# Kernel optimization log

Hardware: AMD Instinct MI355X
Metric: run time of the kernel (lower is better)

## Reference

```python
import jax, jax.numpy as jnp
import numpy as np

B, P, N = 512, 30, 60
S, NV = 14, 5
HID, DE, DO, NT = 64, 5, 6, 2


def _lin(key, out_d, in_d):
    k1, k2 = jax.random.split(key)
    s = 1.0 / np.sqrt(in_d)
    w = jax.random.uniform(k1, (out_d, in_d), minval=-s, maxval=s, dtype=jnp.float32)
    b = jax.random.uniform(k2, (out_d,), minval=-s, maxval=s, dtype=jnp.float32)
    return w, b


def setup_inputs() -> dict:
    key = jax.random.key(0)
    ks = jax.random.split(key, 13)
    inp = {}
    inp['x'] = jax.random.normal(ks[0], (B, P, N), dtype=jnp.float32)
    inp['y'] = jax.random.normal(ks[1], (B, S, NV), dtype=jnp.float32)
    inp['fr1_w'], inp['fr1_b'] = _lin(ks[2], HID, 2 * P)
    inp['fr2_w'], inp['fr2_b'] = _lin(ks[3], HID // 2, HID)
    inp['fr3_w'], inp['fr3_b'] = _lin(ks[4], DE, HID // 2)
    inp['fr1s_w'], inp['fr1s_b'] = _lin(ks[5], HID, S + P)
    inp['fr2s_w'], inp['fr2s_b'] = _lin(ks[6], HID // 2, HID)
    inp['fr3s_w'], inp['fr3s_b'] = _lin(ks[7], DE, HID // 2)
    inp['fo1_w'], inp['fo1_b'] = _lin(ks[8], HID, P + 2 * DE)
    inp['fo2_w'], inp['fo2_b'] = _lin(ks[9], HID // 2, HID)
    inp['fo3_w'], inp['fo3_b'] = _lin(ks[10], DO, HID // 2)
    inp['fcf_w'], inp['fcf_b'] = _lin(ks[11], NT, DO)
    return inp


def _mlp3(h, w1, b1, w2, b2, w3, b3):
    h = jax.nn.relu(h @ w1.T + b1)
    h = jax.nn.relu(h @ w2.T + b2)
    return jax.nn.relu(h @ w3.T + b3)


def reference(x, y, fr1_w, fr1_b, fr2_w, fr2_b, fr3_w, fr3_b,
              fr1s_w, fr1s_b, fr2s_w, fr2s_b, fr3s_w, fr3s_b,
              fo1_w, fo1_b, fo2_w, fo2_b, fo3_w, fo3_b, fcf_w, fcf_b):
    Bb, Pp, Nn = x.shape
    Nv = y.shape[2]
    # edge list equivalent to one-hot Rr/Rs: product(range(N), range(N)), r != s,
    # receiver-major order -> edges with receiver r are the consecutive block of (N-1)
    rs = np.array([(r, s) for r in range(Nn) for s in range(Nn) if r != s])
    r_idx, s_idx = rs[:, 0], rs[:, 1]
    # track-track edges: gather (Rr/Rs matmul) -> [B, Nr, 2P]
    Bm = jnp.concatenate([x[:, :, r_idx], x[:, :, s_idx]], axis=1).transpose(0, 2, 1)
    E = _mlp3(Bm, fr1_w, fr1_b, fr2_w, fr2_b, fr3_w, fr3_b)  # [B, Nr, De]
    # scatter-sum onto receivers (E @ Rr^T): block-structured sum
    Ebar = E.reshape(Bb, Nn, Nn - 1, -1).sum(axis=2)  # [B, N, De]
    # track-SV edges: product(range(N), range(Nv)), node-major order
    k_idx = np.repeat(np.arange(Nn), Nv)
    v_idx = np.tile(np.arange(Nv), Nn)
    Bsv = jnp.concatenate([x[:, :, k_idx], y[:, :, v_idx]], axis=1).transpose(0, 2, 1)  # [B, Nt, P+S]
    Esv = _mlp3(Bsv, fr1s_w, fr1s_b, fr2s_w, fr2s_b, fr3s_w, fr3s_b)  # [B, Nt, De]
    Ebar_sv = Esv.reshape(Bb, Nn, Nv, -1).sum(axis=2)  # [B, N, De]
    # per-node MLP on [x, Ebar, Ebar_sv]
    C = jnp.concatenate([x.transpose(0, 2, 1), Ebar, Ebar_sv], axis=-1)  # [B, N, P+2De]
    O = _mlp3(C, fo1_w, fo1_b, fo2_w, fo2_b, fo3_w, fo3_b)  # [B, N, Do]
    Nsum = O.sum(axis=1)  # [B, Do]
    return jax.nn.relu(Nsum @ fcf_w.T + fcf_b)  # [B, n_targets]
```

## Files before the change

### kernel.cpp

```cpp
#include <hip/hip_runtime.h>

#define BB 512
#define PP 30
#define NN 60
#define SS 14
#define NV 5
#define HID 64
#define HH 32
#define DE 5
#define DO_ 6
#define NT 2
#define CS 40
#define CSP 41
#define HSP 68

typedef __bf16 bf16x8 __attribute__((ext_vector_type(8)));
typedef float  f32x16 __attribute__((ext_vector_type(16)));

union B8u { bf16x8 v; uint4 u; };

__device__ __forceinline__ void unpk2(unsigned int wv, float* f) {
    f[0] = __uint_as_float(wv << 16);
    f[1] = __uint_as_float(wv & 0xffff0000u);
}

__device__ __forceinline__ void load_frags(
    const float* __restrict__ w2p, const float* __restrict__ b2p,
    const float* __restrict__ w3p, const float* __restrict__ b3p,
    int el, int p, bf16x8* af, bf16x8* a2f, float* b2r, float* b3v)
{
    #pragma unroll
    for (int kq = 0; kq < 4; kq++) {
        const float* src = &w2p[el*HID + kq*16 + p*8];
        float4 a = *(const float4*)src;
        float4 c = *(const float4*)(src + 4);
        bf16x8 f;
        f[0]=(__bf16)a.x; f[1]=(__bf16)a.y; f[2]=(__bf16)a.z; f[3]=(__bf16)a.w;
        f[4]=(__bf16)c.x; f[5]=(__bf16)c.y; f[6]=(__bf16)c.z; f[7]=(__bf16)c.w;
        af[kq] = f;
    }
    #pragma unroll
    for (int m = 0; m < 2; m++) {
        bf16x8 f;
        #pragma unroll
        for (int q = 0; q < 8; q++) f[q] = (__bf16)0.f;
        if (el < DE) {
            const float* src = &w3p[el*HH + 4*p + 16*m];
            float4 a = *(const float4*)src;
            float4 c = *(const float4*)(src + 8);
            f[0]=(__bf16)a.x; f[1]=(__bf16)a.y; f[2]=(__bf16)a.z; f[3]=(__bf16)a.w;
            f[4]=(__bf16)c.x; f[5]=(__bf16)c.y; f[6]=(__bf16)c.z; f[7]=(__bf16)c.w;
        }
        a2f[m] = f;
    }
    #pragma unroll
    for (int q = 0; q < 16; q++) b2r[q] = b2p[(q&3) + 8*(q>>2) + 4*p];
    #pragma unroll
    for (int q = 0; q < 4; q++) b3v[q] = p ? (q == 0 ? b3p[4] : 0.f) : b3p[q];
}

__device__ __forceinline__ void load_u(const __bf16* tab, int r, int p, float* uf) {
    #pragma unroll
    for (int kq = 0; kq < 4; kq++) {
        int off = (kq*16 + p*8) ^ ((r & 7) << 3);
        B8u ub; ub.v = *(const bf16x8*)&tab[r*64 + off];
        unpk2(ub.u.x, uf + kq*8);     unpk2(ub.u.y, uf + kq*8 + 2);
        unpk2(ub.u.z, uf + kq*8 + 4); unpk2(ub.u.w, uf + kq*8 + 6);
    }
}

__device__ __forceinline__ void tile_compute(
    const float* uf, const __bf16* vtab, int vn,
    const bf16x8* af, const bf16x8* a2f, const float* b2r, const float* b3v,
    int p, float* out)
{
    f32x16 acc1;
    #pragma unroll
    for (int q = 0; q < 16; q++) acc1[q] = 0.f;
    #pragma unroll
    for (int kq = 0; kq < 4; kq++) {
        int off = (kq*16 + p*8) ^ ((vn & 7) << 3);
        B8u vb; vb.v = *(const bf16x8*)&vtab[vn*64 + off];
        float vf[8];
        unpk2(vb.u.x, vf); unpk2(vb.u.y, vf+2); unpk2(vb.u.z, vf+4); unpk2(vb.u.w, vf+6);
        bf16x8 bf;
        #pragma unroll
        for (int i = 0; i < 8; i++) bf[i] = (__bf16)fmaxf(uf[kq*8 + i] + vf[i], 0.f);
        acc1 = __builtin_amdgcn_mfma_f32_32x32x16_bf16(af[kq], bf, acc1, 0, 0, 0);
    }
    bf16x8 hb0, hb1;
    #pragma unroll
    for (int q = 0; q < 8; q++) hb0[q] = (__bf16)fmaxf(acc1[q]     + b2r[q],     0.f);
    #pragma unroll
    for (int q = 0; q < 8; q++) hb1[q] = (__bf16)fmaxf(acc1[8 + q] + b2r[8 + q], 0.f);
    f32x16 acc2;
    #pragma unroll
    for (int q = 0; q < 16; q++) acc2[q] = 0.f;
    acc2 = __builtin_amdgcn_mfma_f32_32x32x16_bf16(a2f[0], hb0, acc2, 0, 0, 0);
    acc2 = __builtin_amdgcn_mfma_f32_32x32x16_bf16(a2f[1], hb1, acc2, 0, 0, 0);
    #pragma unroll
    for (int q = 0; q < 4; q++) out[q] = fmaxf(acc2[q] + b3v[q], 0.f);
}

__global__ __launch_bounds__(256) void k_fused(
    const float* __restrict__ x, const float* __restrict__ y,
    const float* __restrict__ fr1_w, const float* __restrict__ fr1_b,
    const float* __restrict__ fr2_w, const float* __restrict__ fr2_b,
    const float* __restrict__ fr3_w, const float* __restrict__ fr3_b,
    const float* __restrict__ fr1s_w, const float* __restrict__ fr1s_b,
    const float* __restrict__ fr2s_w, const float* __restrict__ fr2s_b,
    const float* __restrict__ fr3s_w, const float* __restrict__ fr3s_b,
    const float* __restrict__ fo1_w, const float* __restrict__ fo1_b,
    const float* __restrict__ fo2_w, const float* __restrict__ fo2_b,
    const float* __restrict__ fo3_w, const float* __restrict__ fo3_b,
    const float* __restrict__ fcw, const float* __restrict__ fcb,
    float* __restrict__ out)
{
    __shared__ alignas(16) __bf16 uT[NN*64];
    __shared__ alignas(16) __bf16 vT[NN*64];
    __shared__ alignas(16) __bf16 ukT[NN*64];
    __shared__ alignas(16) __bf16 vyT[8*64];
    __shared__ float cl[NN*CSP];
    __shared__ float hl[NN*HSP];
    __shared__ float pl[NN*4*DO_];
    __shared__ float nsum[DO_];

    int b = blockIdx.x, t = threadIdx.x;
    int h = t & 63;
    int w = __builtin_amdgcn_readfirstlane(t >> 6);

    if (t < DO_) nsum[t] = 0.f;
    for (int i = t; i < PP*NN; i += 256) {
        int c = i / NN, n = i - c*NN;
        cl[n*CSP + c] = x[b*PP*NN + i];
    }

    {
        float wu[PP], wv[PP], wk[PP];
        #pragma unroll
        for (int p2 = 0; p2 < PP; p2++) {
            wu[p2] = fr1_w[h*2*PP + p2];
            wv[p2] = fr1_w[h*2*PP + PP + p2];
            wk[p2] = fr1s_w[h*(SS+PP) + p2];
        }
        float b1h = fr1_b[h];
        const float* xb = x + b*PP*NN;
        for (int rr = 0; rr < 15; rr++) {
            int n = w*15 + rr;
            float su = 0.f, sv = 0.f, sk = 0.f;
            #pragma unroll
            for (int p2 = 0; p2 < PP; p2++) {
                float xv = xb[p2*NN + n];
                su += wu[p2]*xv; sv += wv[p2]*xv; sk += wk[p2]*xv;
            }
            int idx = n*64 + (h ^ ((n & 7) << 3));
            uT[idx]  = (__bf16)su;
            vT[idx]  = (__bf16)(sv + b1h);
            ukT[idx] = (__bf16)sk;
        }
        if (w == 0) {
            float wy[SS];
            #pragma unroll
            for (int q = 0; q < SS; q++) wy[q] = fr1s_w[h*(SS+PP) + PP + q];
            float b1s = fr1s_b[h];
            #pragma unroll
            for (int v = 0; v < NV; v++) {
                float s = 0.f;
                #pragma unroll
                for (int q = 0; q < SS; q++) s += wy[q] * y[b*SS*NV + q*NV + v];
                vyT[v*64 + (h ^ (v << 3))] = (__bf16)(s + b1s);
            }
        }
    }
    __syncthreads();

    int p = h >> 5, el = h & 31;
    {
        bf16x8 af[4], a2f[2]; float b2r[16], b3v[4];
        load_frags(fr2_w, fr2_b, fr3_w, fr3_b, el, p, af, a2f, b2r, b3v);
        for (int rr = 0; rr < 15; rr++) {
            int r = w*15 + rr;
            float uf[32];
            load_u(uT, r, p, uf);
            float racc[4] = {0.f, 0.f, 0.f, 0.f};
            #pragma unroll
            for (int half = 0; half < 2; half++) {
                int j0 = half*32 + el;
                int s = j0 + (j0 >= r ? 1 : 0);
                s = s > 59 ? 59 : s;
                bool valid = j0 < 59;
                float val[4];
                tile_compute(uf, vT, s, af, a2f, b2r, b3v, p, val);
                #pragma unroll
                for (int q = 0; q < 4; q++) racc[q] += valid ? val[q] : 0.f;
            }
            #pragma unroll
            for (int q = 0; q < 4; q++) {
                float v2 = racc[q];
                v2 += __shfl_xor(v2, 1);
                v2 += __shfl_xor(v2, 2);
                v2 += __shfl_xor(v2, 4);
                v2 += __shfl_xor(v2, 8);
                v2 += __shfl_xor(v2, 16);
                racc[q] = v2;
            }
            if (el == 0) {
                if (p == 0) {
                    #pragma unroll
                    for (int q = 0; q < 4; q++) cl[r*CSP + PP + q] = racc[q];
                } else {
                    cl[r*CSP + PP + 4] = racc[0];
                }
            }
        }
    }
    {
        bf16x8 af[4], a2f[2]; float b2r[16], b3v[4];
        load_frags(fr2s_w, fr2s_b, fr3s_w, fr3s_b, el, p, af, a2f, b2r, b3v);
        for (int tt = w; tt < 15; tt += 4) {
            int r = tt*4 + (el >> 3);
            int v = el & 7;
            bool valid = v < NV;
            float uf[32];
            load_u(ukT, r, p, uf);
            float val[4];
            tile_compute(uf, vyT, valid ? v : 0, af, a2f, b2r, b3v, p, val);
            #pragma unroll
            for (int q = 0; q < 4; q++) {
                float x2 = valid ? val[q] : 0.f;
                x2 += __shfl_xor(x2, 1);
                x2 += __shfl_xor(x2, 2);
                x2 += __shfl_xor(x2, 4);
                val[q] = x2;
            }
            if ((el & 7) == 0) {
                if (p == 0) {
                    #pragma unroll
                    for (int q = 0; q < 4; q++) cl[r*CSP + PP + DE + q] = val[q];
                } else {
                    cl[r*CSP + PP + DE + 4] = val[0];
                }
            }
        }
    }
    __syncthreads();

    {
        int n = h, rep = w;
        if (n < NN) {
            float c_[CS];
            #pragma unroll
            for (int c = 0; c < CS; c++) c_[c] = cl[n*CSP + c];
            #pragma unroll
            for (int kk = 0; kk < 16; kk++) {
                int k = rep*16 + kk;
                float s = fo1_b[k];
                #pragma unroll
                for (int c = 0; c < CS; c++) s += fo1_w[k*CS + c] * c_[c];
                hl[n*HSP + k] = fmaxf(s, 0.f);
            }
        }
        __syncthreads();
        if (n < NN) {
            float acc[8];
            #pragma unroll
            for (int jj = 0; jj < 8; jj++) acc[jj] = fo2_b[rep*8 + jj];
            for (int kq = 0; kq < HID/4; kq++) {
                float4 h4 = *(const float4*)&hl[n*HSP + kq*4];
                #pragma unroll
                for (int jj = 0; jj < 8; jj++) {
                    const float4 wv4 = *(const float4*)&fo2_w[(rep*8 + jj)*HID + kq*4];
                    acc[jj] += wv4.x*h4.x + wv4.y*h4.y + wv4.z*h4.z + wv4.w*h4.w;
                }
            }
            #pragma unroll
            for (int d = 0; d < DO_; d++) {
                float s = 0.f;
                #pragma unroll
                for (int jj = 0; jj < 8; jj++) s += fo3_w[d*HH + rep*8 + jj] * fmaxf(acc[jj], 0.f);
                pl[(n*4 + rep)*DO_ + d] = s;
            }
        }
        __syncthreads();
        if (t < NN) {
            #pragma unroll
            for (int d = 0; d < DO_; d++) {
                float s = fo3_b[d] + pl[(t*4+0)*DO_+d] + pl[(t*4+1)*DO_+d]
                                   + pl[(t*4+2)*DO_+d] + pl[(t*4+3)*DO_+d];
                atomicAdd(&nsum[d], fmaxf(s, 0.f));
            }
        }
        __syncthreads();
        if (t < NT) {
            float s = fcb[t];
            #pragma unroll
            for (int d = 0; d < DO_; d++) s += fcw[t*DO_ + d] * nsum[d];
            out[b*NT + t] = fmaxf(s, 0.f);
        }
    }
}

extern "C" void kernel_launch(void* const* d_in, const int* in_sizes, int n_in,
                              void* d_out, int out_size, void* d_ws, size_t ws_size,
                              hipStream_t stream)
{
    const float* x      = (const float*)d_in[0];
    const float* y      = (const float*)d_in[1];
    const float* fr1_w  = (const float*)d_in[2];  const float* fr1_b  = (const float*)d_in[3];
    const float* fr2_w  = (const float*)d_in[4];  const float* fr2_b  = (const float*)d_in[5];
    const float* fr3_w  = (const float*)d_in[6];  const float* fr3_b  = (const float*)d_in[7];
    const float* fr1s_w = (const float*)d_in[8];  const float* fr1s_b = (const float*)d_in[9];
    const float* fr2s_w = (const float*)d_in[10]; const float* fr2s_b = (const float*)d_in[11];
    const float* fr3s_w = (const float*)d_in[12]; const float* fr3s_b = (const float*)d_in[13];
    const float* fo1_w  = (const float*)d_in[14]; const float* fo1_b  = (const float*)d_in[15];
    const float* fo2_w  = (const float*)d_in[16]; const float* fo2_b  = (const float*)d_in[17];
    const float* fo3_w  = (const float*)d_in[18]; const float* fo3_b  = (const float*)d_in[19];
    const float* fcf_w  = (const float*)d_in[20]; const float* fcf_b  = (const float*)d_in[21];

    hipLaunchKernelGGL(k_fused, dim3(BB), dim3(256), 0, stream,
                       x, y, fr1_w, fr1_b, fr2_w, fr2_b, fr3_w, fr3_b,
                       fr1s_w, fr1s_b, fr2s_w, fr2s_b, fr3s_w, fr3s_b,
                       fo1_w, fo1_b, fo2_w, fo2_b, fo3_w, fo3_b, fcf_w, fcf_b,
                       (float*)d_out);
}
```

Measured before the change: 164.7 us.

## Switch edge MLP to fp16 packed math and use 8 warps per block

Switches the edge-MLP intermediate tables and MFMA operands from bf16 to fp16. The add+relu of u and v now runs with packed v_pk_add/v_pk_max on half2 instead of unpacking to fp32, and the hidden layer is packed with cvt_pkrtz. The block grows from 256 to 512 threads (8 warps), and the node-MLP work is redistributed with a transposed hl/pl layout. Shared memory is aliased so that hl/pl reuse the u/v/uk tables, which lowers LDS use and raises occupancy. The risk is fp16 range and precision loss versus bf16, plus a different rounding mode.

```diff
diff --git a/kernel.cpp b/kernel.cpp
--- a/kernel.cpp
+++ b/kernel.cpp
@@ -1,4 +1,5 @@
 #include <hip/hip_runtime.h>
+#include <hip/hip_fp16.h>
 
 #define BB 512
 #define PP 30
@@ -12,44 +13,49 @@
 #define NT 2
 #define CS 40
 #define CSP 41
-#define HSP 68
-
-typedef __bf16 bf16x8 __attribute__((ext_vector_type(8)));
-typedef float  f32x16 __attribute__((ext_vector_type(16)));
-
-union B8u { bf16x8 v; uint4 u; };
-
-__device__ __forceinline__ void unpk2(unsigned int wv, float* f) {
-    f[0] = __uint_as_float(wv << 16);
-    f[1] = __uint_as_float(wv & 0xffff0000u);
+#define NW 8
+
+typedef _Float16 f16;
+typedef f16 f16x8 __attribute__((ext_vector_type(8)));
+typedef __fp16 fp16x2 __attribute__((ext_vector_type(2)));
+typedef float f32x16 __attribute__((ext_vector_type(16)));
+
+union H8 { f16x8 v; unsigned u32[4]; uint4 u; };
+union CV { fp16x2 h; unsigned u; };
+
+__device__ __forceinline__ unsigned pk_addrelu(unsigned a, unsigned b) {
+    unsigned s, r;
+    asm("v_pk_add_f16 %0, %1, %2" : "=v"(s) : "v"(a), "v"(b));
+    asm("v_pk_max_f16 %0, %1, 0"  : "=v"(r) : "v"(s));
+    return r;
 }
 
 __device__ __forceinline__ void load_frags(
     const float* __restrict__ w2p, const float* __restrict__ b2p,
     const float* __restrict__ w3p, const float* __restrict__ b3p,
-    int el, int p, bf16x8* af, bf16x8* a2f, float* b2r, float* b3v)
+    int el, int p, f16x8* af, f16x8* a2f, float* b2r, float* b3v)
 {
     #pragma unroll
     for (int kq = 0; kq < 4; kq++) {
         const float* src = &w2p[el*HID + kq*16 + p*8];
         float4 a = *(const float4*)src;
         float4 c = *(const float4*)(src + 4);
-        bf16x8 f;
-        f[0]=(__bf16)a.x; f[1]=(__bf16)a.y; f[2]=(__bf16)a.z; f[3]=(__bf16)a.w;
-        f[4]=(__bf16)c.x; f[5]=(__bf16)c.y; f[6]=(__bf16)c.z; f[7]=(__bf16)c.w;
+        f16x8 f;
+        f[0]=(f16)a.x; f[1]=(f16)a.y; f[2]=(f16)a.z; f[3]=(f16)a.w;
+        f[4]=(f16)c.x; f[5]=(f16)c.y; f[6]=(f16)c.z; f[7]=(f16)c.w;
         af[kq] = f;
     }
     #pragma unroll
     for (int m = 0; m < 2; m++) {
-        bf16x8 f;
+        f16x8 f;
         #pragma unroll
-        for (int q = 0; q < 8; q++) f[q] = (__bf16)0.f;
+        for (int q = 0; q < 8; q++) f[q] = (f16)0.f;
         if (el < DE) {
             const float* src = &w3p[el*HH + 4*p + 16*m];
             float4 a = *(const float4*)src;
             float4 c = *(const float4*)(src + 8);
-            f[0]=(__bf16)a.x; f[1]=(__bf16)a.y; f[2]=(__bf16)a.z; f[3]=(__bf16)a.w;
-            f[4]=(__bf16)c.x; f[5]=(__bf16)c.y; f[6]=(__bf16)c.z; f[7]=(__bf16)c.w;
+            f[0]=(f16)a.x; f[1]=(f16)a.y; f[2]=(f16)a.z; f[3]=(f16)a.w;
+            f[4]=(f16)c.x; f[5]=(f16)c.y; f[6]=(f16)c.z; f[7]=(f16)c.w;
         }
         a2f[m] = f;
     }
@@ -59,19 +65,17 @@
     for (int q = 0; q < 4; q++) b3v[q] = p ? (q == 0 ? b3p[4] : 0.f) : b3p[q];
 }
 
-__device__ __forceinline__ void load_u(const __bf16* tab, int r, int p, float* uf) {
+__device__ __forceinline__ void load_u(const __half* tab, int r, int p, H8* u8) {
     #pragma unroll
     for (int kq = 0; kq < 4; kq++) {
         int off = (kq*16 + p*8) ^ ((r & 7) << 3);
-        B8u ub; ub.v = *(const bf16x8*)&tab[r*64 + off];
-        unpk2(ub.u.x, uf + kq*8);     unpk2(ub.u.y, uf + kq*8 + 2);
-        unpk2(ub.u.z, uf + kq*8 + 4); unpk2(ub.u.w, uf + kq*8 + 6);
+        u8[kq].u = *(const uint4*)&tab[r*64 + off];
     }
 }
 
 __device__ __forceinline__ void tile_compute(
-    const float* uf, const __bf16* vtab, int vn,
-    const bf16x8* af, const bf16x8* a2f, const float* b2r, const float* b3v,
+    const H8* u8, const __half* vtab, int vn,
+    const f16x8* af, const f16x8* a2f, const float* b2r, const float* b3v,
     int p, float* out)
 {
     f32x16 acc1;
@@ -80,29 +84,33 @@
     #pragma unroll
     for (int kq = 0; kq < 4; kq++) {
         int off = (kq*16 + p*8) ^ ((vn & 7) << 3);
-        B8u vb; vb.v = *(const bf16x8*)&vtab[vn*64 + off];
-        float vf[8];
-        unpk2(vb.u.x, vf); unpk2(vb.u.y, vf+2); unpk2(vb.u.z, vf+4); unpk2(vb.u.w, vf+6);
-        bf16x8 bf;
+        H8 vb; vb.u = *(const uint4*)&vtab[vn*64 + off];
+        H8 hb;
         #pragma unroll
-        for (int i = 0; i < 8; i++) bf[i] = (__bf16)fmaxf(uf[kq*8 + i] + vf[i], 0.f);
-        acc1 = __builtin_amdgcn_mfma_f32_32x32x16_bf16(af[kq], bf, acc1, 0, 0, 0);
-    }
-    bf16x8 hb0, hb1;
-    #pragma unroll
-    for (int q = 0; q < 8; q++) hb0[q] = (__bf16)fmaxf(acc1[q]     + b2r[q],     0.f);
-    #pragma unroll
-    for (int q = 0; q < 8; q++) hb1[q] = (__bf16)fmaxf(acc1[8 + q] + b2r[8 + q], 0.f);
+        for (int j = 0; j < 4; j++) hb.u32[j] = pk_addrelu(u8[kq].u32[j], vb.u32[j]);
+        acc1 = __builtin_amdgcn_mfma_f32_32x32x16_f16(af[kq], hb.v, acc1, 0, 0, 0);
+    }
+    H8 hb0, hb1;
+    #pragma unroll
+    for (int i = 0; i < 4; i++) {
+        CV c0, c1;
+        c0.h = __builtin_amdgcn_cvt_pkrtz(fmaxf(acc1[2*i]   + b2r[2*i],   0.f),
+                                          fmaxf(acc1[2*i+1] + b2r[2*i+1], 0.f));
+        c1.h = __builtin_amdgcn_cvt_pkrtz(fmaxf(acc1[8+2*i]   + b2r[8+2*i],   0.f),
+                                          fmaxf(acc1[8+2*i+1] + b2r[8+2*i+1], 0.f));
+        hb0.u32[i] = c0.u;
+        hb1.u32[i] = c1.u;
+    }
     f32x16 acc2;
     #pragma unroll
     for (int q = 0; q < 16; q++) acc2[q] = 0.f;
-    acc2 = __builtin_amdgcn_mfma_f32_32x32x16_bf16(a2f[0], hb0, acc2, 0, 0, 0);
-    acc2 = __builtin_amdgcn_mfma_f32_32x32x16_bf16(a2f[1], hb1, acc2, 0, 0, 0);
+    acc2 = __builtin_amdgcn_mfma_f32_32x32x16_f16(a2f[0], hb0.v, acc2, 0, 0, 0);
+    acc2 = __builtin_amdgcn_mfma_f32_32x32x16_f16(a2f[1], hb1.v, acc2, 0, 0, 0);
     #pragma unroll
     for (int q = 0; q < 4; q++) out[q] = fmaxf(acc2[q] + b3v[q], 0.f);
 }
 
-__global__ __launch_bounds__(256) void k_fused(
+__global__ __launch_bounds__(512, 4) void k_fused(
     const float* __restrict__ x, const float* __restrict__ y,
     const float* __restrict__ fr1_w, const float* __restrict__ fr1_b,
     const float* __restrict__ fr2_w, const float* __restrict__ fr2_b,
@@ -116,13 +124,14 @@
     const float* __restrict__ fcw, const float* __restrict__ fcb,
     float* __restrict__ out)
 {
-    __shared__ alignas(16) __bf16 uT[NN*64];
-    __shared__ alignas(16) __bf16 vT[NN*64];
-    __shared__ alignas(16) __bf16 ukT[NN*64];
-    __shared__ alignas(16) __bf16 vyT[8*64];
+    __shared__ alignas(16) char smem[26880];
+    __half* uT  = (__half*)smem;
+    __half* vT  = (__half*)(smem + 7680);
+    __half* ukT = (__half*)(smem + 15360);
+    float*  hl  = (float*)smem;
+    float*  pl  = (float*)(smem + 15360);
+    __shared__ alignas(16) __half vyT[8*64];
     __shared__ float cl[NN*CSP];
-    __shared__ float hl[NN*HSP];
-    __shared__ float pl[NN*4*DO_];
     __shared__ float nsum[DO_];
 
     int b = blockIdx.x, t = threadIdx.x;
@@ -130,7 +139,7 @@
     int w = __builtin_amdgcn_readfirstlane(t >> 6);
 
     if (t < DO_) nsum[t] = 0.f;
-    for (int i = t; i < PP*NN; i += 256) {
+    for (int i = t; i < PP*NN; i += 512) {
         int c = i / NN, n = i - c*NN;
         cl[n*CSP + c] = x[b*PP*NN + i];
     }
@@ -145,8 +154,7 @@
         }
         float b1h = fr1_b[h];
         const float* xb = x + b*PP*NN;
-        for (int rr = 0; rr < 15; rr++) {
-            int n = w*15 + rr;
+        for (int n = w; n < NN; n += NW) {
             float su = 0.f, sv = 0.f, sk = 0.f;
             #pragma unroll
             for (int p2 = 0; p2 < PP; p2++) {
@@ -154,9 +162,9 @@
                 su += wu[p2]*xv; sv += wv[p2]*xv; sk += wk[p2]*xv;
             }
             int idx = n*64 + (h ^ ((n & 7) << 3));
-            uT[idx]  = (__bf16)su;
-            vT[idx]  = (__bf16)(sv + b1h);
-            ukT[idx] = (__bf16)sk;
+            uT[idx]  = (__half)su;
+            vT[idx]  = (__half)(sv + b1h);
+            ukT[idx] = (__half)sk;
         }
         if (w == 0) {
             float wy[SS];
@@ -168,7 +176,7 @@
                 float s = 0.f;
                 #pragma unroll
                 for (int q = 0; q < SS; q++) s += wy[q] * y[b*SS*NV + q*NV + v];
-                vyT[v*64 + (h ^ (v << 3))] = (__bf16)(s + b1s);
+                vyT[v*64 + (h ^ (v << 3))] = (__half)(s + b1s);
             }
         }
     }
@@ -176,12 +184,11 @@
 
     int p = h >> 5, el = h & 31;
     {
-        bf16x8 af[4], a2f[2]; float b2r[16], b3v[4];
+        f16x8 af[4], a2f[2]; float b2r[16], b3v[4];
         load_frags(fr2_w, fr2_b, fr3_w, fr3_b, el, p, af, a2f, b2r, b3v);
-        for (int rr = 0; rr < 15; rr++) {
-            int r = w*15 + rr;
-            float uf[32];
-            load_u(uT, r, p, uf);
+        for (int r = w; r < NN; r += NW) {
+            H8 u8[4];
+            load_u(uT, r, p, u8);
             float racc[4] = {0.f, 0.f, 0.f, 0.f};
             #pragma unroll
             for (int half = 0; half < 2; half++) {
@@ -190,7 +197,7 @@
                 s = s > 59 ? 59 : s;
                 bool valid = j0 < 59;
                 float val[4];
-                tile_compute(uf, vT, s, af, a2f, b2r, b3v, p, val);
+                tile_compute(u8, vT, s, af, a2f, b2r, b3v, p, val);
                 #pragma unroll
                 for (int q = 0; q < 4; q++) racc[q] += valid ? val[q] : 0.f;
             }
@@ -215,16 +222,16 @@
         }
     }
     {
-        bf16x8 af[4], a2f[2]; float b2r[16], b3v[4];
+        f16x8 af[4], a2f[2]; float b2r[16], b3v[4];
         load_frags(fr2s_w, fr2s_b, fr3s_w, fr3s_b, el, p, af, a2f, b2r, b3v);
-        for (int tt = w; tt < 15; tt += 4) {
+        for (int tt = w; tt < 15; tt += NW) {
             int r = tt*4 + (el >> 3);
             int v = el & 7;
             bool valid = v < NV;
-            float uf[32];
-            load_u(ukT, r, p, uf);
+            H8 u8[4];
+            load_u(ukT, r, p, u8);
             float val[4];
-            tile_compute(uf, vyT, valid ? v : 0, af, a2f, b2r, b3v, p, val);
+            tile_compute(u8, vyT, valid ? v : 0, af, a2f, b2r, b3v, p, val);
             #pragma unroll
             for (int q = 0; q < 4; q++) {
                 float x2 = valid ? val[q] : 0.f;
@@ -246,47 +253,45 @@
     __syncthreads();
 
     {
-        int n = h, rep = w;
+        int n = h;
         if (n < NN) {
             float c_[CS];
             #pragma unroll
             for (int c = 0; c < CS; c++) c_[c] = cl[n*CSP + c];
             #pragma unroll
-            for (int kk = 0; kk < 16; kk++) {
-                int k = rep*16 + kk;
+            for (int kk = 0; kk < 8; kk++) {
+                int k = w*8 + kk;
                 float s = fo1_b[k];
                 #pragma unroll
                 for (int c = 0; c < CS; c++) s += fo1_w[k*CS + c] * c_[c];
-                hl[n*HSP + k] = fmaxf(s, 0.f);
+                hl[k*NN + n] = fmaxf(s, 0.f);
             }
         }
         __syncthreads();
         if (n < NN) {
-            float acc[8];
-            #pragma unroll
-            for (int jj = 0; jj < 8; jj++) acc[jj] = fo2_b[rep*8 + jj];
-            for (int kq = 0; kq < HID/4; kq++) {
-                float4 h4 = *(const float4*)&hl[n*HSP + kq*4];
-                #pragma unroll
-                for (int jj = 0; jj < 8; jj++) {
-                    const float4 wv4 = *(const float4*)&fo2_w[(rep*8 + jj)*HID + kq*4];
-                    acc[jj] += wv4.x*h4.x + wv4.y*h4.y + wv4.z*h4.z + wv4.w*h4.w;
-                }
+            float acc[4];
+            #pragma unroll
+            for (int jj = 0; jj < 4; jj++) acc[jj] = fo2_b[w*4 + jj];
+            for (int k = 0; k < HID; k++) {
+                float hv = hl[k*NN + n];
+                #pragma unroll
+                for (int jj = 0; jj < 4; jj++) acc[jj] += fo2_w[(w*4 + jj)*HID + k] * hv;
             }
             #pragma unroll
             for (int d = 0; d < DO_; d++) {
                 float s = 0.f;
                 #pragma unroll
-                for (int jj = 0; jj < 8; jj++) s += fo3_w[d*HH + rep*8 + jj] * fmaxf(acc[jj], 0.f);
-                pl[(n*4 + rep)*DO_ + d] = s;
+                for (int jj = 0; jj < 4; jj++) s += fo3_w[d*HH + w*4 + jj] * fmaxf(acc[jj], 0.f);
+                pl[(w*DO_ + d)*NN + n] = s;
             }
         }
         __syncthreads();
         if (t < NN) {
             #pragma unroll
             for (int d = 0; d < DO_; d++) {
-                float s = fo3_b[d] + pl[(t*4+0)*DO_+d] + pl[(t*4+1)*DO_+d]
-                                   + pl[(t*4+2)*DO_+d] + pl[(t*4+3)*DO_+d];
+                float s = fo3_b[d];
+                #pragma unroll
+                for (int g = 0; g < NW; g++) s += pl[(g*DO_ + d)*NN + t];
                 atomicAdd(&nsum[d], fmaxf(s, 0.f));
             }
         }
@@ -317,7 +322,7 @@
     const float* fo3_w  = (const float*)d_in[18]; const float* fo3_b  = (const float*)d_in[19];
     const float* fcf_w  = (const float*)d_in[20]; const float* fcf_b  = (const float*)d_in[21];
 
-    hipLaunchKernelGGL(k_fused, dim3(BB), dim3(256), 0, stream,
+    hipLaunchKernelGGL(k_fused, dim3(BB), dim3(512), 0, stream,
                        x, y, fr1_w, fr1_b, fr2_w, fr2_b, fr3_w, fr3_b,
                        fr1s_w, fr1s_b, fr2s_w, fr2s_b, fr3s_w, fr3s_b,
                        fo1_w, fo1_b, fo2_w, fo2_b, fo3_w, fo3_b, fcf_w, fcf_b,
```

New measurement: 142.7 us. 1.15x faster.
